# Optimization experiments

Hardware: AMD Instinct MI355X
Metric: run time of the kernel (lower is better)

The kernel has to match this reference:

```python
import jax, jax.numpy as jnp
import numpy as np

B, S, D, H, DH = 8, 1024, 768, 12, 64
INIT_STD = 0.02
IGNORE = -100000.0


def setup_inputs() -> dict:
    key = jax.random.key(0)
    ks = jax.random.split(key, 5)
    return {
        "normalized_resid_pre": jax.random.normal(ks[0], (B, S, D), dtype=jnp.float32),
        "W_Q": jax.random.normal(ks[1], (H, D, DH), dtype=jnp.float32) * INIT_STD,
        "b_Q": jnp.zeros((H, DH), dtype=jnp.float32),
        "W_K": jax.random.normal(ks[2], (H, D, DH), dtype=jnp.float32) * INIT_STD,
        "b_K": jnp.zeros((H, DH), dtype=jnp.float32),
        "W_V": jax.random.normal(ks[3], (H, D, DH), dtype=jnp.float32) * INIT_STD,
        "b_V": jnp.zeros((H, DH), dtype=jnp.float32),
        "W_O": jax.random.normal(ks[4], (H, DH, D), dtype=jnp.float32) * INIT_STD,
        "b_O": jnp.zeros((D,), dtype=jnp.float32),
    }


def reference(normalized_resid_pre, W_Q, b_Q, W_K, b_K, W_V, b_V, W_O, b_O):
    x = normalized_resid_pre  # [B,S,D]
    q = jnp.einsum('bsd,hde->bshe', x, W_Q) + b_Q  # [B,S,H,DH]
    k = jnp.einsum('bsd,hde->bshe', x, W_K) + b_K
    v = jnp.einsum('bsd,hde->bshe', x, W_V) + b_V
    scores = jnp.einsum('bqhe,bkhe->bhqk', q, k) / jnp.sqrt(jnp.float32(DH))
    causal = jnp.triu(jnp.ones((S, S), dtype=bool), k=1)  # True above diagonal
    scores = jnp.where(causal, jnp.float32(IGNORE), scores)
    pattern = jax.nn.softmax(scores, axis=-1)  # [B,H,S,S]
    z = jnp.einsum('bhqk,bkhe->bqhe', pattern, v)  # [B,S,H,DH]
    attn_out = jnp.einsum('bqhe,hed->bqd', z, W_O) + b_O  # [B,S,D]
    return attn_out
```

## Files before the change

### kernel.cpp

```cpp
#include <hip/hip_runtime.h>
#include <hip/hip_bf16.h>
#include <stdint.h>

#define BB 8
#define SS 1024
#define DD 768
#define HH 12
#define DHH 64
#define BS (BB*SS)
#define NQKV (3*HH*DHH)

typedef __attribute__((ext_vector_type(8))) short bf16x8;
typedef __attribute__((ext_vector_type(4))) float f32x4;
typedef __attribute__((ext_vector_type(4))) unsigned int u32x4;

typedef const __attribute__((address_space(1))) unsigned int gu32;
typedef __attribute__((address_space(3))) unsigned int lu32;

static __device__ __forceinline__ unsigned short f2bf(float f) {
    union { float f; unsigned int u; } v; v.f = f;
    unsigned int u = v.u;
    unsigned int r = (u + 0x7fffu + ((u >> 16) & 1u)) >> 16;
    return (unsigned short)r;
}

static __device__ __forceinline__ unsigned int cvt_pk_bf16(float lo, float hi) {
    unsigned int r;
    asm("v_cvt_pk_bf16_f32 %0, %1, %2" : "=v"(r) : "v"(lo), "v"(hi));
    return r;
}

#define WB2() asm volatile("s_waitcnt vmcnt(2)\ns_barrier" ::: "memory")
#define WB0() asm volatile("s_waitcnt vmcnt(0)\ns_barrier" ::: "memory")


__global__ void k_prep(const float* __restrict__ x,
                       const float* __restrict__ wq, const float* __restrict__ wk,
                       const float* __restrict__ wv, const float* __restrict__ wo,
                       unsigned short* __restrict__ xb,
                       unsigned short* __restrict__ wt,
                       unsigned short* __restrict__ wot) {
    __shared__ float tl[64][65];
    int id = blockIdx.x;
    int t = threadIdx.x;
    if (id < 6144) {
        int i = (id * 256 + t) * 4;
        float4 v = *reinterpret_cast<const float4*>(x + i);
        ushort4 o;
        o.x = f2bf(v.x); o.y = f2bf(v.y); o.z = f2bf(v.z); o.w = f2bf(v.w);
        *reinterpret_cast<ushort4*>(xb + i) = o;
        return;
    }
    int row = t >> 4, c4 = (t & 15) * 4;
    if (id < 6576) {
        int q = id - 6144;
        int rt = q % 12, z = q / 12;
        int mat = z / 12, h = z - mat * 12;
        const float* src = ((mat == 0) ? wq : (mat == 1) ? wk : wv) + (size_t)h * 768 * 64;
        int d0 = rt * 64;
        #pragma unroll
        for (int p = 0; p < 4; ++p) {
            int d = p * 16 + row;
            float4 v = *reinterpret_cast<const float4*>(&src[(size_t)(d0 + d) * 64 + c4]);
            tl[d][c4 + 0] = v.x; tl[d][c4 + 1] = v.y; tl[d][c4 + 2] = v.z; tl[d][c4 + 3] = v.w;
        }
        __syncthreads();
        unsigned short* dstb = wt + ((size_t)(mat * 768 + h * 64)) * 768;
        #pragma unroll
        for (int p = 0; p < 4; ++p) {
            int e = p * 16 + row;
            ushort4 o;
            o.x = f2bf(tl[c4 + 0][e]); o.y = f2bf(tl[c4 + 1][e]);
            o.z = f2bf(tl[c4 + 2][e]); o.w = f2bf(tl[c4 + 3][e]);
            *reinterpret_cast<ushort4*>(&dstb[(size_t)e * 768 + d0 + c4]) = o;
        }
        return;
    }
    {
        int q = id - 6576;
        int r0 = (q % 12) * 64;
        int c0 = (q / 12) * 64;
        #pragma unroll
        for (int p = 0; p < 4; ++p) {
            int r = p * 16 + row;
            float4 v = *reinterpret_cast<const float4*>(&wo[(size_t)(r0 + r) * 768 + c0 + c4]);
            tl[r][c4 + 0] = v.x; tl[r][c4 + 1] = v.y; tl[r][c4 + 2] = v.z; tl[r][c4 + 3] = v.w;
        }
        __syncthreads();
        #pragma unroll
        for (int p = 0; p < 4; ++p) {
            int c = p * 16 + row;
            ushort4 o;
            o.x = f2bf(tl[c4 + 0][c]); o.y = f2bf(tl[c4 + 1][c]);
            o.z = f2bf(tl[c4 + 2][c]); o.w = f2bf(tl[c4 + 3][c]);
            *reinterpret_cast<ushort4*>(&wot[(size_t)(c0 + c) * 768 + r0 + c4]) = o;
        }
    }
}

__global__ void k_transpose_v(const unsigned short* __restrict__ vb, unsigned short* __restrict__ vtb) {
    __shared__ unsigned short tl[64][68];
    int s0 = blockIdx.x * 64;
    int bh = blockIdx.y;
    const unsigned short* src = vb + (size_t)bh * SS * DHH;
    unsigned short* dst = vtb + (size_t)bh * DHH * SS;
    int t = threadIdx.x;
    int r16 = t >> 4;
    int c4 = (t & 15) * 4;
    #pragma unroll
    for (int p = 0; p < 4; ++p) {
        int sl = p * 16 + r16;
        ushort4 v = *reinterpret_cast<const ushort4*>(&src[(size_t)(s0 + sl) * DHH + c4]);
        *reinterpret_cast<ushort4*>(&tl[sl][c4]) = v;
    }
    __syncthreads();
    #pragma unroll
    for (int p = 0; p < 4; ++p) {
        int e = p * 16 + r16;
        ushort4 o;
        o.x = tl[c4 + 0][e]; o.y = tl[c4 + 1][e];
        o.z = tl[c4 + 2][e]; o.w = tl[c4 + 3][e];
        *reinterpret_cast<ushort4*>(&dst[(size_t)e * SS + s0 + c4]) = o;
    }
}


__launch_bounds__(256)
__global__ void k_gemm_qkv(const unsigned short* __restrict__ xb,
                           const unsigned short* __restrict__ wt,
                           const float* __restrict__ bq, const float* __restrict__ bk,
                           const float* __restrict__ bv,
                           unsigned short* __restrict__ qb,
                           unsigned short* __restrict__ kb,
                           unsigned short* __restrict__ vb) {
    __shared__ unsigned short As[128 * 32];
    __shared__ unsigned short Bs[128 * 32];
    int r0 = blockIdx.x * 128;
    int c0 = blockIdx.y * 128;
    int t = threadIdx.x;
    int w = t >> 6, l = t & 63;
    int lr = l & 15, lg = l >> 4;
    int wr = w >> 1, wc = w & 1;
    int srow = l >> 2, sko = (l & 3) * 8;

    f32x4 acc[4][4] = {};
    for (int k0 = 0; k0 < DD; k0 += 32) {
        __syncthreads();
        #pragma unroll
        for (int c = 0; c < 2; ++c) {
            int seg = w * 2 + c;
            int row = seg * 16 + srow;
            __builtin_amdgcn_global_load_lds(
                (gu32*)(xb + (size_t)(r0 + row) * DD + k0 + sko),
                (lu32*)&As[seg * 512], 16, 0, 0);
            __builtin_amdgcn_global_load_lds(
                (gu32*)(wt + (size_t)(c0 + row) * DD + k0 + sko),
                (lu32*)&Bs[seg * 512], 16, 0, 0);
        }
        __syncthreads();
        bf16x8 af[4], bfr[4];
        #pragma unroll
        for (int m = 0; m < 4; ++m)
            af[m] = *reinterpret_cast<const bf16x8*>(&As[(wr * 64 + m * 16 + lr) * 32 + lg * 8]);
        #pragma unroll
        for (int n = 0; n < 4; ++n)
            bfr[n] = *reinterpret_cast<const bf16x8*>(&Bs[(wc * 64 + n * 16 + lr) * 32 + lg * 8]);
        #pragma unroll
        for (int m = 0; m < 4; ++m)
            #pragma unroll
            for (int n = 0; n < 4; ++n)
                acc[m][n] = __builtin_amdgcn_mfma_f32_16x16x32_bf16(af[m], bfr[n], acc[m][n], 0, 0, 0);
    }
    #pragma unroll
    for (int n = 0; n < 4; ++n) {
        int c = c0 + wc * 64 + n * 16 + lr;
        int mat = c / 768;
        int within = c - mat * 768;
        int h = within >> 6, e = within & 63;
        const float* bptr = (mat == 0) ? bq : (mat == 1) ? bk : bv;
        float bias = bptr[within];
        unsigned short* dst = (mat == 0) ? qb : (mat == 1) ? kb : vb;
        #pragma unroll
        for (int m = 0; m < 4; ++m) {
            #pragma unroll
            for (int i = 0; i < 4; ++i) {
                int r = r0 + wr * 64 + m * 16 + lg * 4 + i;
                int b_ = r >> 10, s_ = r & 1023;
                dst[(((size_t)(b_ * HH + h)) * SS + s_) * DHH + e] = f2bf(acc[m][n][i] + bias);
            }
        }
    }
}


#define PW 34

__launch_bounds__(256, 4)
__global__ void k_attn(const unsigned short* __restrict__ qb,
                       const unsigned short* __restrict__ kb,
                       const unsigned short* __restrict__ vtb,
                       unsigned short* __restrict__ zb) {
    __shared__ unsigned short Ks[2][64 * 64];
    __shared__ unsigned short Vs[64 * 64];
    __shared__ unsigned int Pl[4][16 * PW];
    int id = blockIdx.x;
    int xcd = id & 7;
    int j = id >> 3;
    int bh = xcd * 12 + (j % 12);
    int qi = 15 - (j / 12);
    int q0 = qi * 64;

    int t = threadIdx.x, w = t >> 6, l = t & 63;
    int lr = l & 15, lg = l >> 4;
    const unsigned short* Qh = qb + (size_t)bh * SS * DHH;
    const unsigned short* Kh = kb + (size_t)bh * SS * DHH;
    const unsigned short* Vt = vtb + (size_t)bh * DHH * SS;
    int b_ = bh / HH, h = bh - b_ * HH;
    unsigned int* Pw = &Pl[w][0];

    int sr8 = l >> 3;
    int sc = ((l & 7) ^ sr8) * 8;

    auto STAGE_K = [&](int buf, int kbase) {
        #pragma unroll
        for (int c = 0; c < 2; ++c) {
            int seg = w * 2 + c;
            int row = seg * 8 + sr8;
            __builtin_amdgcn_global_load_lds(
                (gu32*)(Kh + (size_t)(kbase + row) * DHH + sc),
                (lu32*)&Ks[buf][seg * 512], 16, 0, 0);
        }
    };
    auto STAGE_V = [&](int kbase) {
        #pragma unroll
        for (int c = 0; c < 2; ++c) {
            int seg = w * 2 + c;
            int row = seg * 8 + sr8;
            __builtin_amdgcn_global_load_lds(
                (gu32*)(Vt + (size_t)row * SS + kbase + sc),
                (lu32*)&Vs[seg * 512], 16, 0, 0);
        }
    };

    int qabs = q0 + w * 16 + lr;
    STAGE_K(0, 0);
    bf16x8 qf[2];
    qf[0] = *reinterpret_cast<const bf16x8*>(Qh + (size_t)qabs * DHH + lg * 8);
    qf[1] = *reinterpret_cast<const bf16x8*>(Qh + (size_t)qabs * DHH + 32 + lg * 8);

    float m_r = -3.0e38f, l_r = 0.f;
    f32x4 zacc[4] = {};
    __syncthreads();

    for (int kt = 0; kt <= qi; ++kt) {
        int k0 = kt * 64;
        int cur = kt & 1;
        STAGE_V(k0);
        if (kt < qi) STAGE_K(cur ^ 1, k0 + 64);

        f32x4 sac[4] = {};
        __builtin_amdgcn_s_setprio(1);
        #pragma unroll
        for (int ks = 0; ks < 2; ++ks) {
            #pragma unroll
            for (int ct = 0; ct < 4; ++ct) {
                bf16x8 kfr = *reinterpret_cast<const bf16x8*>(
                    &Ks[cur][(ct * 16 + lr) * 64 + (((ks * 4 + lg) ^ (lr & 7)) * 8)]);
                sac[ct] = __builtin_amdgcn_mfma_f32_16x16x32_bf16(kfr, qf[ks], sac[ct], 0, 0, 0);
            }
        }
        __builtin_amdgcn_s_setprio(0);
        bool diag = (kt == qi);
        float sv[4][4];
        float pm = -3.0e38f;
        #pragma unroll
        for (int ct = 0; ct < 4; ++ct) {
            #pragma unroll
            for (int i = 0; i < 4; ++i) {
                float x = sac[ct][i] * 0.125f;
                if (diag) {
                    int kabs = k0 + ct * 16 + lg * 4 + i;
                    if (kabs > qabs) x = -3.0e38f;
                }
                sv[ct][i] = x;
                pm = fmaxf(pm, x);
            }
        }
        pm = fmaxf(pm, __shfl_xor(pm, 16));
        pm = fmaxf(pm, __shfl_xor(pm, 32));

        if (!__all(pm <= m_r + 8.f)) {
            float mn = fmaxf(m_r, pm);
            float alpha = __expf(m_r - mn);
            m_r = mn;
            l_r *= alpha;
            float aC[4];
            #pragma unroll
            for (int i = 0; i < 4; ++i) aC[i] = __shfl(alpha, lg * 4 + i);
            #pragma unroll
            for (int et = 0; et < 4; ++et)
                #pragma unroll
                for (int i = 0; i < 4; ++i) zacc[et][i] *= aC[i];
        }

        float ps = 0.f;
        #pragma unroll
        for (int ct = 0; ct < 4; ++ct) {
            float p0 = __expf(sv[ct][0] - m_r);
            float p1 = __expf(sv[ct][1] - m_r);
            float p2 = __expf(sv[ct][2] - m_r);
            float p3 = __expf(sv[ct][3] - m_r);
            ps += (p0 + p1) + (p2 + p3);
            unsigned int pk0 = cvt_pk_bf16(p0, p1);
            unsigned int pk1 = cvt_pk_bf16(p2, p3);
            *reinterpret_cast<uint2*>(&Pw[lr * PW + ct * 8 + lg * 2]) = make_uint2(pk0, pk1);
        }
        ps += __shfl_xor(ps, 16);
        ps += __shfl_xor(ps, 32);
        l_r += ps;

        if (kt < qi) WB2(); else WB0();

        __builtin_amdgcn_s_setprio(1);
        #pragma unroll
        for (int ks = 0; ks < 2; ++ks) {
            bf16x8 pa = *reinterpret_cast<const bf16x8*>(&Pw[lr * PW + ks * 16 + lg * 4]);
            #pragma unroll
            for (int et = 0; et < 4; ++et) {
                bf16x8 vf = *reinterpret_cast<const bf16x8*>(
                    &Vs[(et * 16 + lr) * 64 + (((ks * 4 + lg) ^ (lr & 7)) * 8)]);
                zacc[et] = __builtin_amdgcn_mfma_f32_16x16x32_bf16(pa, vf, zacc[et], 0, 0, 0);
            }
        }
        __builtin_amdgcn_s_setprio(0);
        if (kt < qi) __syncthreads();
    }

    float lC[4];
    #pragma unroll
    for (int i = 0; i < 4; ++i) lC[i] = __shfl(l_r, lg * 4 + i);
    #pragma unroll
    for (int et = 0; et < 4; ++et) {
        #pragma unroll
        for (int i = 0; i < 4; ++i) {
            int r = q0 + w * 16 + lg * 4 + i;
            float z = zacc[et][i] / lC[i];
            zb[((size_t)(b_ * SS + r)) * DD + h * DHH + et * 16 + lr] = f2bf(z);
        }
    }
}


__launch_bounds__(256)
__global__ void k_gemm_out(const unsigned short* __restrict__ zb,
                           const unsigned short* __restrict__ wot,
                           const float* __restrict__ bo,
                           float* __restrict__ out) {
    __shared__ unsigned short As[128 * 32];
    __shared__ unsigned short Bs[128 * 32];
    int r0 = blockIdx.x * 128;
    int c0 = blockIdx.y * 128;
    int t = threadIdx.x;
    int w = t >> 6, l = t & 63;
    int lr = l & 15, lg = l >> 4;
    int wr = w >> 1, wc = w & 1;
    int srow = l >> 2, sko = (l & 3) * 8;

    f32x4 acc[4][4] = {};
    for (int k0 = 0; k0 < DD; k0 += 32) {
        __syncthreads();
        #pragma unroll
        for (int c = 0; c < 2; ++c) {
            int seg = w * 2 + c;
            int row = seg * 16 + srow;
            __builtin_amdgcn_global_load_lds(
                (gu32*)(zb + (size_t)(r0 + row) * DD + k0 + sko),
                (lu32*)&As[seg * 512], 16, 0, 0);
            __builtin_amdgcn_global_load_lds(
                (gu32*)(wot + (size_t)(c0 + row) * DD + k0 + sko),
                (lu32*)&Bs[seg * 512], 16, 0, 0);
        }
        __syncthreads();
        bf16x8 af[4], bfr[4];
        #pragma unroll
        for (int m = 0; m < 4; ++m)
            af[m] = *reinterpret_cast<const bf16x8*>(&As[(wr * 64 + m * 16 + lr) * 32 + lg * 8]);
        #pragma unroll
        for (int n = 0; n < 4; ++n)
            bfr[n] = *reinterpret_cast<const bf16x8*>(&Bs[(wc * 64 + n * 16 + lr) * 32 + lg * 8]);
        #pragma unroll
        for (int m = 0; m < 4; ++m)
            #pragma unroll
            for (int n = 0; n < 4; ++n)
                acc[m][n] = __builtin_amdgcn_mfma_f32_16x16x32_bf16(af[m], bfr[n], acc[m][n], 0, 0, 0);
    }
    #pragma unroll
    for (int n = 0; n < 4; ++n) {
        int c = c0 + wc * 64 + n * 16 + lr;
        float bias = bo[c];
        #pragma unroll
        for (int m = 0; m < 4; ++m) {
            #pragma unroll
            for (int i = 0; i < 4; ++i) {
                int r = r0 + wr * 64 + m * 16 + lg * 4 + i;
                out[(size_t)r * DD + c] = acc[m][n][i] + bias;
            }
        }
    }
}


extern "C" void kernel_launch(void* const* d_in, const int* in_sizes, int n_in,
                              void* d_out, int out_size, void* d_ws, size_t ws_size,
                              hipStream_t stream) {
    const float* x  = (const float*)d_in[0];
    const float* wq = (const float*)d_in[1];
    const float* bq = (const float*)d_in[2];
    const float* wk = (const float*)d_in[3];
    const float* bk = (const float*)d_in[4];
    const float* wv = (const float*)d_in[5];
    const float* bv = (const float*)d_in[6];
    const float* wo = (const float*)d_in[7];
    const float* bo = (const float*)d_in[8];
    float* out = (float*)d_out;

    char* ws = (char*)d_ws;
    size_t off = 0;
    auto alloc = [&](size_t bytes) -> char* {
        char* p = ws + off;
        off += (bytes + 255) & ~(size_t)255;
        return p;
    };
    unsigned short* xb   = (unsigned short*)alloc((size_t)BS * DD * 2);
    unsigned short* wt   = (unsigned short*)alloc((size_t)NQKV * DD * 2);
    unsigned short* wot  = (unsigned short*)alloc((size_t)DD * DD * 2);
    unsigned short* qb   = (unsigned short*)alloc((size_t)BB * HH * SS * DHH * 2);
    unsigned short* kb   = (unsigned short*)alloc((size_t)BB * HH * SS * DHH * 2);
    unsigned short* vb   = (unsigned short*)alloc((size_t)BB * HH * SS * DHH * 2);
    unsigned short* vtb  = (unsigned short*)alloc((size_t)BB * HH * SS * DHH * 2);
    unsigned short* zb   = (unsigned short*)alloc((size_t)BS * DD * 2);
    (void)ws_size; (void)in_sizes; (void)n_in; (void)out_size;

    k_prep<<<dim3(6720), dim3(256), 0, stream>>>(x, wq, wk, wv, wo, xb, wt, wot);
    k_gemm_qkv<<<dim3(BS / 128, NQKV / 128), dim3(256), 0, stream>>>(xb, wt, bq, bk, bv, qb, kb, vb);
    k_transpose_v<<<dim3(SS / 64, BB * HH), dim3(256), 0, stream>>>(vb, vtb);
    k_attn<<<dim3(16 * 96), dim3(256), 0, stream>>>(qb, kb, vtb, zb);
    k_gemm_out<<<dim3(BS / 128, DD / 128), dim3(256), 0, stream>>>(zb, wot, bo, out);
}
```

Baseline: 120.8 us.

## Double-buffer per-wave LDS tiles in projection GEMMs, drop block barriers, swizzle LDS

Both projection GEMMs (QKV and output) now give each wave its own private double-buffered LDS copy of its 64-row A and B slices. Loads for the next k-step are issued before computing the current one, with vmcnt waits in place of the two __syncthreads per iteration. An XOR-style swizzle on the global-to-LDS column offset and the matching read offset is meant to avoid LDS bank conflicts. The cost is twice the global loads, since A and B rows are duplicated across waves, and more LDS use per block, which may reduce occupancy.

```diff
diff --git a/kernel.cpp b/kernel.cpp
--- a/kernel.cpp
+++ b/kernel.cpp
@@ -30,6 +30,8 @@
     return r;
 }
 
+#define VMW8() asm volatile("s_waitcnt vmcnt(8)" ::: "memory")
+#define VMW0() asm volatile("s_waitcnt vmcnt(0)" ::: "memory")
 #define WB2() asm volatile("s_waitcnt vmcnt(2)\ns_barrier" ::: "memory")
 #define WB0() asm volatile("s_waitcnt vmcnt(0)\ns_barrier" ::: "memory")
 
@@ -133,44 +135,59 @@
                            unsigned short* __restrict__ qb,
                            unsigned short* __restrict__ kb,
                            unsigned short* __restrict__ vb) {
-    __shared__ unsigned short As[128 * 32];
-    __shared__ unsigned short Bs[128 * 32];
+    __shared__ unsigned short As[4][2][64 * 32];
+    __shared__ unsigned short Bs[4][2][64 * 32];
     int r0 = blockIdx.x * 128;
     int c0 = blockIdx.y * 128;
     int t = threadIdx.x;
     int w = t >> 6, l = t & 63;
     int lr = l & 15, lg = l >> 4;
     int wr = w >> 1, wc = w & 1;
-    int srow = l >> 2, sko = (l & 3) * 8;
+    int srow = l >> 2;
+    int g8 = (((l & 3) - (l >> 3)) & 3) * 8;
+    int rdo = ((lg + (lr >> 1)) & 3) * 8;
+
+    const unsigned short* Abase = xb + (size_t)(r0 + wr * 64) * DD;
+    const unsigned short* Bbase = wt + (size_t)(c0 + wc * 64) * DD;
 
     f32x4 acc[4][4] = {};
-    for (int k0 = 0; k0 < DD; k0 += 32) {
-        __syncthreads();
-        #pragma unroll
-        for (int c = 0; c < 2; ++c) {
-            int seg = w * 2 + c;
-            int row = seg * 16 + srow;
-            __builtin_amdgcn_global_load_lds(
-                (gu32*)(xb + (size_t)(r0 + row) * DD + k0 + sko),
-                (lu32*)&As[seg * 512], 16, 0, 0);
-            __builtin_amdgcn_global_load_lds(
-                (gu32*)(wt + (size_t)(c0 + row) * DD + k0 + sko),
-                (lu32*)&Bs[seg * 512], 16, 0, 0);
-        }
-        __syncthreads();
+
+    auto STAGE = [&](int buf, int k0) {
+        #pragma unroll
+        for (int i = 0; i < 4; ++i) {
+            int row = i * 16 + srow;
+            __builtin_amdgcn_global_load_lds(
+                (gu32*)(Abase + (size_t)row * DD + k0 + g8),
+                (lu32*)&As[w][buf][i * 512], 16, 0, 0);
+            __builtin_amdgcn_global_load_lds(
+                (gu32*)(Bbase + (size_t)row * DD + k0 + g8),
+                (lu32*)&Bs[w][buf][i * 512], 16, 0, 0);
+        }
+    };
+    auto COMPUTE = [&](int buf) {
         bf16x8 af[4], bfr[4];
         #pragma unroll
         for (int m = 0; m < 4; ++m)
-            af[m] = *reinterpret_cast<const bf16x8*>(&As[(wr * 64 + m * 16 + lr) * 32 + lg * 8]);
+            af[m] = *reinterpret_cast<const bf16x8*>(&As[w][buf][(m * 16 + lr) * 32 + rdo]);
         #pragma unroll
         for (int n = 0; n < 4; ++n)
-            bfr[n] = *reinterpret_cast<const bf16x8*>(&Bs[(wc * 64 + n * 16 + lr) * 32 + lg * 8]);
+            bfr[n] = *reinterpret_cast<const bf16x8*>(&Bs[w][buf][(n * 16 + lr) * 32 + rdo]);
         #pragma unroll
         for (int m = 0; m < 4; ++m)
             #pragma unroll
             for (int n = 0; n < 4; ++n)
                 acc[m][n] = __builtin_amdgcn_mfma_f32_16x16x32_bf16(af[m], bfr[n], acc[m][n], 0, 0, 0);
-    }
+    };
+
+    STAGE(0, 0);
+    for (int i = 0; i < 11; ++i) {
+        int kb2 = i * 64;
+        STAGE(1, kb2 + 32); VMW8(); COMPUTE(0);
+        STAGE(0, kb2 + 64); VMW8(); COMPUTE(1);
+    }
+    STAGE(1, 736); VMW8(); COMPUTE(0);
+    VMW0(); COMPUTE(1);
+
     #pragma unroll
     for (int n = 0; n < 4; ++n) {
         int c = c0 + wc * 64 + n * 16 + lr;
@@ -356,44 +373,59 @@
                            const unsigned short* __restrict__ wot,
                            const float* __restrict__ bo,
                            float* __restrict__ out) {
-    __shared__ unsigned short As[128 * 32];
-    __shared__ unsigned short Bs[128 * 32];
+    __shared__ unsigned short As[4][2][64 * 32];
+    __shared__ unsigned short Bs[4][2][64 * 32];
     int r0 = blockIdx.x * 128;
     int c0 = blockIdx.y * 128;
     int t = threadIdx.x;
     int w = t >> 6, l = t & 63;
     int lr = l & 15, lg = l >> 4;
     int wr = w >> 1, wc = w & 1;
-    int srow = l >> 2, sko = (l & 3) * 8;
+    int srow = l >> 2;
+    int g8 = (((l & 3) - (l >> 3)) & 3) * 8;
+    int rdo = ((lg + (lr >> 1)) & 3) * 8;
+
+    const unsigned short* Abase = zb + (size_t)(r0 + wr * 64) * DD;
+    const unsigned short* Bbase = wot + (size_t)(c0 + wc * 64) * DD;
 
     f32x4 acc[4][4] = {};
-    for (int k0 = 0; k0 < DD; k0 += 32) {
-        __syncthreads();
-        #pragma unroll
-        for (int c = 0; c < 2; ++c) {
-            int seg = w * 2 + c;
-            int row = seg * 16 + srow;
-            __builtin_amdgcn_global_load_lds(
-                (gu32*)(zb + (size_t)(r0 + row) * DD + k0 + sko),
-                (lu32*)&As[seg * 512], 16, 0, 0);
-            __builtin_amdgcn_global_load_lds(
-                (gu32*)(wot + (size_t)(c0 + row) * DD + k0 + sko),
-                (lu32*)&Bs[seg * 512], 16, 0, 0);
-        }
-        __syncthreads();
+
+    auto STAGE = [&](int buf, int k0) {
+        #pragma unroll
+        for (int i = 0; i < 4; ++i) {
+            int row = i * 16 + srow;
+            __builtin_amdgcn_global_load_lds(
+                (gu32*)(Abase + (size_t)row * DD + k0 + g8),
+                (lu32*)&As[w][buf][i * 512], 16, 0, 0);
+            __builtin_amdgcn_global_load_lds(
+                (gu32*)(Bbase + (size_t)row * DD + k0 + g8),
+                (lu32*)&Bs[w][buf][i * 512], 16, 0, 0);
+        }
+    };
+    auto COMPUTE = [&](int buf) {
         bf16x8 af[4], bfr[4];
         #pragma unroll
         for (int m = 0; m < 4; ++m)
-            af[m] = *reinterpret_cast<const bf16x8*>(&As[(wr * 64 + m * 16 + lr) * 32 + lg * 8]);
+            af[m] = *reinterpret_cast<const bf16x8*>(&As[w][buf][(m * 16 + lr) * 32 + rdo]);
         #pragma unroll
         for (int n = 0; n < 4; ++n)
-            bfr[n] = *reinterpret_cast<const bf16x8*>(&Bs[(wc * 64 + n * 16 + lr) * 32 + lg * 8]);
+            bfr[n] = *reinterpret_cast<const bf16x8*>(&Bs[w][buf][(n * 16 + lr) * 32 + rdo]);
         #pragma unroll
         for (int m = 0; m < 4; ++m)
             #pragma unroll
             for (int n = 0; n < 4; ++n)
                 acc[m][n] = __builtin_amdgcn_mfma_f32_16x16x32_bf16(af[m], bfr[n], acc[m][n], 0, 0, 0);
-    }
+    };
+
+    STAGE(0, 0);
+    for (int i = 0; i < 11; ++i) {
+        int kb2 = i * 64;
+        STAGE(1, kb2 + 32); VMW8(); COMPUTE(0);
+        STAGE(0, kb2 + 64); VMW8(); COMPUTE(1);
+    }
+    STAGE(1, 736); VMW8(); COMPUTE(0);
+    VMW0(); COMPUTE(1);
+
     #pragma unroll
     for (int n = 0; n < 4; ++n) {
         int c = c0 + wc * 64 + n * 16 + lr;
```

New measurement: 137.3 us. 13.7% more time.
